# Kernel tuning notes

Hardware: AMD Instinct MI355X
Metric: run time of the kernel (lower is better)

## Reference

```python
import jax, jax.numpy as jnp
import numpy as np

H = 64  # latent_dim // 2


def _lstm_cell(x, h, c, Wih, Whh, b):
    # PyTorch gate order: i, f, g, o
    g = x @ Wih.T + h @ Whh.T + b
    i, f, gg, o = jnp.split(g, 4, axis=-1)
    c = jax.nn.sigmoid(f) * c + jax.nn.sigmoid(i) * jnp.tanh(gg)
    h = jax.nn.sigmoid(o) * jnp.tanh(c)
    return h, c


def _run_lstm(x, Wih, Whh, b):
    # x: [B, T, D] -> outputs [B, T, H], final h, c (zero-initialized state)
    B = x.shape[0]
    h0 = jnp.zeros((B, Whh.shape[1]), x.dtype)

    def step(carry, xt):
        h, c = _lstm_cell(xt, carry[0], carry[1], Wih, Whh, b)
        return (h, c), h

    (h, c), ys = jax.lax.scan(step, (h0, h0), jnp.swapaxes(x, 0, 1))
    return jnp.swapaxes(ys, 0, 1), h, c


def setup_inputs() -> dict:
    key = jax.random.key(0)
    ks = jax.random.split(key, 16)
    B, S, T, D = 512, 1024, 512, 3
    s = 1.0 / np.sqrt(H)

    def u(k, shape):
        return jax.random.uniform(k, shape, jnp.float32, -s, s)

    return {
        "src": jax.random.normal(ks[0], (B, S, D), jnp.float32),
        "trg": jax.random.normal(ks[1], (B, T, D), jnp.float32),
        "enc1_Wih": u(ks[2], (4 * H, D)),
        "enc1_Whh": u(ks[3], (4 * H, H)),
        "enc1_b": u(ks[4], (4 * H,)),
        "enc2_Wih": u(ks[5], (4 * H, H)),
        "enc2_Whh": u(ks[6], (4 * H, H)),
        "enc2_b": u(ks[7], (4 * H,)),
        "dec1_Wih": u(ks[8], (4 * H, D)),
        "dec1_Whh": u(ks[9], (4 * H, H)),
        "dec1_b": u(ks[10], (4 * H,)),
        "dec2_Wih": u(ks[11], (4 * H, H)),
        "dec2_Whh": u(ks[12], (4 * H, H)),
        "dec2_b": u(ks[13], (4 * H,)),
        "fc_W": u(ks[14], (D, H)),
        "fc_b": u(ks[15], (D,)),
    }


def reference(src, trg, enc1_Wih, enc1_Whh, enc1_b, enc2_Wih, enc2_Whh, enc2_b,
              dec1_Wih, dec1_Whh, dec1_b, dec2_Wih, dec2_Whh, dec2_b, fc_W, fc_b):
    # Encoder: two stacked LSTMs over src; keep final state of layer 2.
    y1, _, _ = _run_lstm(src, enc1_Wih, enc1_Whh, enc1_b)
    _, h, c = _run_lstm(y1, enc2_Wih, enc2_Whh, enc2_b)

    # Decoder (teacher_forcing_ratio = 1.0, the only well-defined branch):
    # at each step both decoder LSTMs share/chain the SAME (h, c) state,
    # exactly as the original Decoder.forward does with seq-len-1 inputs.
    def step(carry, xt):
        h, c = carry
        h1, c1 = _lstm_cell(xt, h, c, dec1_Wih, dec1_Whh, dec1_b)
        h2, c2 = _lstm_cell(h1, h1, c1, dec2_Wih, dec2_Whh, dec2_b)
        return (h2, c2), h2 @ fc_W.T + fc_b

    xs = jnp.swapaxes(trg[:, :-1, :], 0, 1)  # inputs for t = 1..T-1
    _, preds = jax.lax.scan(step, (h, c), xs)
    preds = jnp.swapaxes(preds, 0, 1)  # [B, T-1, 3]

    B = trg.shape[0]
    zero0 = jnp.zeros((B, 1, fc_b.shape[0]), preds.dtype)  # outputs[:, 0] stays 0
    return jnp.concatenate([zero0, preds], axis=1)
```

## Files before the change

### kernel.cpp

```cpp
#include <hip/hip_runtime.h>
#include <math.h>

typedef _Float16 f16;
typedef _Float16 f16x8 __attribute__((ext_vector_type(8)));
typedef float    f32x4 __attribute__((ext_vector_type(4)));

#define MFMA16(A, B, C) __builtin_amdgcn_mfma_f32_16x16x32_f16((A), (B), (C), 0, 0, 0)
#define LOG2E 1.44269504088896f

__device__ __forceinline__ float sig2(float a) {
    return __builtin_amdgcn_rcpf(1.0f + __builtin_amdgcn_exp2f(a));
}
__device__ __forceinline__ float tanh2(float c) {
    return fmaf(2.0f, sig2(c * (-2.0f * LOG2E)), -1.0f);
}

__device__ __forceinline__ f16x8 ldfrag(const float* __restrict__ W, int n, int k0, float s) {
    const float* p = W + (size_t)n * 64 + k0;
    f16x8 r;
#pragma unroll
    for (int j = 0; j < 8; j++) r[j] = (f16)(s * p[j]);
    return r;
}

__global__ __launch_bounds__(512, 2)
void seq2seq_kernel(const float* __restrict__ src, const float* __restrict__ trg,
                    const float* __restrict__ e1ih, const float* __restrict__ e1hh,
                    const float* __restrict__ e1b,
                    const float* __restrict__ e2ih, const float* __restrict__ e2hh,
                    const float* __restrict__ e2b,
                    const float* __restrict__ d1ih, const float* __restrict__ d1hh,
                    const float* __restrict__ d1b,
                    const float* __restrict__ d2ih, const float* __restrict__ d2hh,
                    const float* __restrict__ d2b,
                    const float* __restrict__ fcW, const float* __restrict__ fcb,
                    float* __restrict__ out)
{
    const int bp   = blockIdx.x;
    const int tid  = threadIdx.x;
    const int wv   = tid >> 6;
    const bool isB = (wv >= 4);
    const int wvg  = wv & 3;
    const int lane = tid & 63;
    const int quad = lane >> 4;
    const int c15  = lane & 15;
    const int u16  = wvg * 16 + c15;
    const int qb   = quad & 1;
    const int ab   = c15 & 1;

    __shared__ __align__(16) float xst[1024][8];
    __shared__ __align__(16) float tst[512][8];
    __shared__ __align__(16) f16 h1l[2][2][64];
    __shared__ __align__(16) f16 h2l[2][2][64];
    __shared__ float c1buf[2][64];
    __shared__ float c2buf[2][64];
    __shared__ __align__(16) f16 ring[2][16][72];

    {
        const float* s0 = src + (size_t)(2 * bp) * 3072;
        const float* s1 = s0 + 3072;
        for (int i = tid; i < 3072; i += 512) {
            int t = i / 3, c = i - 3 * t;
            xst[t][c]     = s0[i];
            xst[t][4 + c] = s1[i];
        }
        const float* t0p = trg + (size_t)(2 * bp) * 1536;
        const float* t1p = t0p + 1536;
        for (int i = tid; i < 1536; i += 512) {
            int t = i / 3, c = i - 3 * t;
            tst[t][c]     = t0p[i];
            tst[t][4 + c] = t1p[i];
        }
    }

    f16x8 E1hh[4][2];
    f16x8 E2ih[4][2], E2hh[4][2];
    float xw[4][3], bias1[4];
    f32x4 bs2[4];
    if (!isB) {
#pragma unroll
        for (int g = 0; g < 4; g++) {
            const float s = (g == 2) ? (-2.0f * LOG2E) : (-LOG2E);
            const int n = g * 64 + u16;
#pragma unroll
            for (int c = 0; c < 2; c++)
                E1hh[g][c] = ldfrag(e1hh, n, c * 32 + quad * 8, s);
            xw[g][0] = s * e1ih[n * 3 + 0];
            xw[g][1] = s * e1ih[n * 3 + 1];
            xw[g][2] = s * e1ih[n * 3 + 2];
            bias1[g] = s * e1b[n];
        }
    } else {
#pragma unroll
        for (int g = 0; g < 4; g++) {
            const float s = (g == 2) ? (-2.0f * LOG2E) : (-LOG2E);
            const int n = g * 64 + u16;
#pragma unroll
            for (int c = 0; c < 2; c++) {
                E2ih[g][c] = ldfrag(e2ih, n, c * 32 + quad * 8, s);
                E2hh[g][c] = ldfrag(e2hh, n, c * 32 + quad * 8, s);
            }
            float bv = s * e2b[n];
            bs2[g] = (f32x4){bv, bv, bv, bv};
        }
    }

    float c1 = 0.f, c2 = 0.f;
    if (tid < 256) {
        (&h1l[0][0][0])[tid] = (f16)0.f;
        (&h2l[0][0][0])[tid] = (f16)0.f;
    }
    __syncthreads();

    const f32x4 z4 = {0.f, 0.f, 0.f, 0.f};

    f32x4 xq = z4, xnq = z4;
    if (!isB) xq = *(const f32x4*)&xst[0][qb * 4];

#pragma unroll 1
    for (int tau = 0; tau <= 1024; tau++) {
        const int w = tau & 1;
        if (!isB) {
            if (tau < 1024) {
                const f16* h1p = h1l[w ^ 1][ab];
                f16x8 a0 = *(const f16x8*)(h1p + quad * 8);
                f16x8 a1 = *(const f16x8*)(h1p + 32 + quad * 8);
                float xt[4];
#pragma unroll
                for (int g = 0; g < 4; g++)
                    xt[g] = fmaf(xw[g][0], xq.x,
                            fmaf(xw[g][1], xq.y, fmaf(xw[g][2], xq.z, bias1[g])));
                f32x4 acc[4];
#pragma unroll
                for (int g = 0; g < 4; g++)
                    acc[g] = MFMA16(a1, E1hh[g][1], MFMA16(a0, E1hh[g][0], z4));
                float v[4];
#pragma unroll
                for (int g = 0; g < 4; g++)
                    v[g] = (qb ? acc[g][1] : acc[g][0]) + xt[g];
                float iv = sig2(v[0]), fv = sig2(v[1]);
                float gv = fmaf(2.0f, sig2(v[2]), -1.0f), ov = sig2(v[3]);
                c1 = fv * c1 + iv * gv;
                if (quad < 2) h1l[w][quad][u16] = (f16)(ov * tanh2(c1));
                const int tn = (tau + 1 < 1024) ? tau + 1 : 1023;
                xnq = *(const f32x4*)&xst[tn][qb * 4];
            }
        } else {
            if (tau > 0) {
                const f16* h1p = h1l[w ^ 1][ab];
                const f16* h2p = h2l[w ^ 1][ab];
                f16x8 a0 = *(const f16x8*)(h1p + quad * 8);
                f16x8 a1 = *(const f16x8*)(h1p + 32 + quad * 8);
                f16x8 b0 = *(const f16x8*)(h2p + quad * 8);
                f16x8 b1 = *(const f16x8*)(h2p + 32 + quad * 8);
                f32x4 accA[4], accB[4];
#pragma unroll
                for (int g = 0; g < 4; g++) {
                    accA[g] = MFMA16(a1, E2ih[g][1], MFMA16(a0, E2ih[g][0], bs2[g]));
                    accB[g] = MFMA16(b1, E2hh[g][1], MFMA16(b0, E2hh[g][0], z4));
                }
                float v[4];
#pragma unroll
                for (int g = 0; g < 4; g++)
                    v[g] = (qb ? accA[g][1] : accA[g][0]) +
                           (qb ? accB[g][1] : accB[g][0]);
                float iv = sig2(v[0]), fv = sig2(v[1]);
                float gv = fmaf(2.0f, sig2(v[2]), -1.0f), ov = sig2(v[3]);
                c2 = fv * c2 + iv * gv;
                if (quad < 2) h2l[w][quad][u16] = (f16)(ov * tanh2(c2));
            }
        }
        __syncthreads();
        if (!isB) xq = xnq;
    }

    f16x8 D1hh[4][2];
    f16x8 W2s[4][2];
    float dxw[4][3], db1[4];
    f32x4 db2s[4];
    if (!isB) {
#pragma unroll
        for (int g = 0; g < 4; g++) {
            const float s = (g == 2) ? (-2.0f * LOG2E) : (-LOG2E);
            const int n = g * 64 + u16;
#pragma unroll
            for (int c = 0; c < 2; c++)
                D1hh[g][c] = ldfrag(d1hh, n, c * 32 + quad * 8, s);
            dxw[g][0] = s * d1ih[n * 3 + 0];
            dxw[g][1] = s * d1ih[n * 3 + 1];
            dxw[g][2] = s * d1ih[n * 3 + 2];
            db1[g] = s * d1b[n];
        }
    } else {
#pragma unroll
        for (int g = 0; g < 4; g++) {
            const float s = (g == 2) ? (-2.0f * LOG2E) : (-LOG2E);
            const int n = g * 64 + u16;
#pragma unroll
            for (int c = 0; c < 2; c++) {
                const int k0 = c * 32 + quad * 8;
                const float* pa = d2ih + (size_t)n * 64 + k0;
                const float* pb = d2hh + (size_t)n * 64 + k0;
                f16x8 r;
#pragma unroll
                for (int j = 0; j < 8; j++) r[j] = (f16)(s * (pa[j] + pb[j]));
                W2s[g][c] = r;
            }
            float bv = s * d2b[n];
            db2s[g] = (f32x4){bv, bv, bv, bv};
        }
        if (quad < 2) c2buf[quad][u16] = c2;
    }
    f16x8 FW0 = {}, FW1 = {};
    float fb = 0.f;
    if (wv >= 6 && c15 < 3) {
#pragma unroll
        for (int j = 0; j < 8; j++) {
            FW0[j] = (f16)fcW[c15 * 64 + quad * 8 + j];
            FW1[j] = (f16)fcW[c15 * 64 + 32 + quad * 8 + j];
        }
        fb = fcb[c15];
    }
    __syncthreads();

    f32x4 tq = z4, tnq = z4;
    if (!isB) tq = *(const f32x4*)&tst[0][qb * 4];

#pragma unroll 1
    for (int t = 0; t < 511; t++) {
        const int r = t & 1, w = r ^ 1;
        if (!isB) {
            const f16* hp = h2l[r][ab];
            f16x8 a0 = *(const f16x8*)(hp + quad * 8);
            f16x8 a1 = *(const f16x8*)(hp + 32 + quad * 8);
            float cdin = c2buf[qb][u16];
            float xt[4];
#pragma unroll
            for (int g = 0; g < 4; g++)
                xt[g] = fmaf(dxw[g][0], tq.x,
                        fmaf(dxw[g][1], tq.y, fmaf(dxw[g][2], tq.z, db1[g])));
            f32x4 acc[4];
#pragma unroll
            for (int g = 0; g < 4; g++)
                acc[g] = MFMA16(a1, D1hh[g][1], MFMA16(a0, D1hh[g][0], z4));
            float v[4];
#pragma unroll
            for (int g = 0; g < 4; g++)
                v[g] = (qb ? acc[g][1] : acc[g][0]) + xt[g];
            float iv = sig2(v[0]), fv = sig2(v[1]);
            float gv = fmaf(2.0f, sig2(v[2]), -1.0f), ov = sig2(v[3]);
            float c1d = fv * cdin + iv * gv;
            if (quad < 2) {
                h1l[w][quad][u16] = (f16)(ov * tanh2(c1d));
                c1buf[quad][u16]  = c1d;
            }
            const int tn = (t + 1 < 511) ? t + 1 : 510;
            tnq = *(const f32x4*)&tst[tn][qb * 4];
        } else if (wv >= 6 && t > 0 && (t & 15) == 0) {
            const int bsel = wv - 6;
            const f16* rp = &ring[bsel][0][0];
            f16x8 fa0 = *(const f16x8*)(rp + c15 * 72 + quad * 8);
            f16x8 fa1 = *(const f16x8*)(rp + c15 * 72 + 32 + quad * 8);
            f32x4 acc = MFMA16(fa1, FW1, MFMA16(fa0, FW0, z4));
            if (c15 < 3) {
                float* ob = out + (((size_t)(2 * bp + bsel) * 512 + (t - 15)) * 3) + c15;
#pragma unroll
                for (int rg = 0; rg < 4; rg++)
                    ob[(quad * 4 + rg) * 3] = acc[rg] + fb;
            }
        }
        __syncthreads();
        if (!isB) tq = tnq;

        if (isB) {
            const f16* np = h1l[w][ab];
            f16x8 m0 = *(const f16x8*)(np + quad * 8);
            f16x8 m1 = *(const f16x8*)(np + 32 + quad * 8);
            float c1in = c1buf[qb][u16];
            f32x4 acc[4];
#pragma unroll
            for (int g = 0; g < 4; g++)
                acc[g] = MFMA16(m1, W2s[g][1], MFMA16(m0, W2s[g][0], db2s[g]));
            float v[4];
#pragma unroll
            for (int g = 0; g < 4; g++)
                v[g] = (qb ? acc[g][1] : acc[g][0]);
            float i2 = sig2(v[0]), f2 = sig2(v[1]);
            float g2 = fmaf(2.0f, sig2(v[2]), -1.0f), o2 = sig2(v[3]);
            float c2d = f2 * c1in + i2 * g2;
            if (quad < 2) {
                f16 hh = (f16)(o2 * tanh2(c2d));
                h2l[w][quad][u16] = hh;
                c2buf[quad][u16]  = c2d;
                ring[quad][t & 15][u16] = hh;
            }
        }
        __syncthreads();
    }

    if (wv >= 6) {
        const int bsel = wv - 6;
        const f16* rp = &ring[bsel][0][0];
        f16x8 fa0 = *(const f16x8*)(rp + c15 * 72 + quad * 8);
        f16x8 fa1 = *(const f16x8*)(rp + c15 * 72 + 32 + quad * 8);
        f32x4 acc = MFMA16(fa1, FW1, MFMA16(fa0, FW0, z4));
        if (c15 < 3) {
            float* ob = out + (((size_t)(2 * bp + bsel) * 512 + 497) * 3) + c15;
#pragma unroll
            for (int rg = 0; rg < 4; rg++) {
                int step = quad * 4 + rg;
                if (step < 15) ob[step * 3] = acc[rg] + fb;
            }
        }
    }
}

extern "C" void kernel_launch(void* const* d_in, const int* in_sizes, int n_in,
                              void* d_out, int out_size, void* d_ws, size_t ws_size,
                              hipStream_t stream)
{
    const float* src   = (const float*)d_in[0];
    const float* trg   = (const float*)d_in[1];
    const float* e1ih  = (const float*)d_in[2];
    const float* e1hh  = (const float*)d_in[3];
    const float* e1b   = (const float*)d_in[4];
    const float* e2ih  = (const float*)d_in[5];
    const float* e2hh  = (const float*)d_in[6];
    const float* e2b   = (const float*)d_in[7];
    const float* dd1ih = (const float*)d_in[8];
    const float* dd1hh = (const float*)d_in[9];
    const float* dd1b  = (const float*)d_in[10];
    const float* dd2ih = (const float*)d_in[11];
    const float* dd2hh = (const float*)d_in[12];
    const float* dd2b  = (const float*)d_in[13];
    const float* fcW   = (const float*)d_in[14];
    const float* fcb   = (const float*)d_in[15];
    float* out = (float*)d_out;

    hipMemsetAsync(d_out, 0, (size_t)out_size * sizeof(float), stream);

    seq2seq_kernel<<<256, 512, 0, stream>>>(src, trg,
                                            e1ih, e1hh, e1b, e2ih, e2hh, e2b,
                                            dd1ih, dd1hh, dd1b, dd2ih, dd2hh, dd2b,
                                            fcW, fcb, out);
}
```

Baseline: 832.3 us.

## Move encoder layer-2 input projection to layer-1 waves via shared-memory pipeline

Encoder layer-1 waves now also compute the layer-2 input projection (h1 times E2ih) and pass it to the layer-2 waves through a double-buffered shared buffer. This adds one pipeline stage and one extra loop iteration. Layer-2 waves then run only the recurrent MFMAs, which balances the per-step work between the two wave groups and shortens the critical path per barrier. Launch bounds drop to one block per SM to give room for the extra register fragments, and the h2 buffer parity in the decoder is flipped to match the new final write index.

```diff
diff --git a/kernel.cpp b/kernel.cpp
--- a/kernel.cpp
+++ b/kernel.cpp
@@ -23,7 +23,7 @@
     return r;
 }
 
-__global__ __launch_bounds__(512, 2)
+__global__ __launch_bounds__(512, 1)
 void seq2seq_kernel(const float* __restrict__ src, const float* __restrict__ trg,
                     const float* __restrict__ e1ih, const float* __restrict__ e1hh,
                     const float* __restrict__ e1b,
@@ -55,6 +55,7 @@
     __shared__ float c1buf[2][64];
     __shared__ float c2buf[2][64];
     __shared__ __align__(16) f16 ring[2][16][72];
+    __shared__ __align__(16) float prj[2][2][64][4];
 
     {
         const float* s0 = src + (size_t)(2 * bp) * 3072;
@@ -73,8 +74,8 @@
         }
     }
 
-    f16x8 E1hh[4][2];
-    f16x8 E2ih[4][2], E2hh[4][2];
+    f16x8 E1hh[4][2], E2ih[4][2];
+    f16x8 E2hh[4][2];
     float xw[4][3], bias1[4];
     f32x4 bs2[4];
     if (!isB) {
@@ -83,8 +84,10 @@
             const float s = (g == 2) ? (-2.0f * LOG2E) : (-LOG2E);
             const int n = g * 64 + u16;
 #pragma unroll
-            for (int c = 0; c < 2; c++)
+            for (int c = 0; c < 2; c++) {
                 E1hh[g][c] = ldfrag(e1hh, n, c * 32 + quad * 8, s);
+                E2ih[g][c] = ldfrag(e2ih, n, c * 32 + quad * 8, s);
+            }
             xw[g][0] = s * e1ih[n * 3 + 0];
             xw[g][1] = s * e1ih[n * 3 + 1];
             xw[g][2] = s * e1ih[n * 3 + 2];
@@ -96,10 +99,8 @@
             const float s = (g == 2) ? (-2.0f * LOG2E) : (-LOG2E);
             const int n = g * 64 + u16;
 #pragma unroll
-            for (int c = 0; c < 2; c++) {
-                E2ih[g][c] = ldfrag(e2ih, n, c * 32 + quad * 8, s);
+            for (int c = 0; c < 2; c++)
                 E2hh[g][c] = ldfrag(e2hh, n, c * 32 + quad * 8, s);
-            }
             float bv = s * e2b[n];
             bs2[g] = (f32x4){bv, bv, bv, bv};
         }
@@ -118,56 +119,65 @@
     if (!isB) xq = *(const f32x4*)&xst[0][qb * 4];
 
 #pragma unroll 1
-    for (int tau = 0; tau <= 1024; tau++) {
-        const int w = tau & 1;
+    for (int tau = 0; tau <= 1025; tau++) {
         if (!isB) {
-            if (tau < 1024) {
-                const f16* h1p = h1l[w ^ 1][ab];
+            if (tau <= 1024) {
+                const f16* h1p = h1l[(tau + 1) & 1][ab];
                 f16x8 a0 = *(const f16x8*)(h1p + quad * 8);
                 f16x8 a1 = *(const f16x8*)(h1p + 32 + quad * 8);
-                float xt[4];
-#pragma unroll
-                for (int g = 0; g < 4; g++)
-                    xt[g] = fmaf(xw[g][0], xq.x,
-                            fmaf(xw[g][1], xq.y, fmaf(xw[g][2], xq.z, bias1[g])));
-                f32x4 acc[4];
-#pragma unroll
-                for (int g = 0; g < 4; g++)
-                    acc[g] = MFMA16(a1, E1hh[g][1], MFMA16(a0, E1hh[g][0], z4));
-                float v[4];
-#pragma unroll
-                for (int g = 0; g < 4; g++)
-                    v[g] = (qb ? acc[g][1] : acc[g][0]) + xt[g];
-                float iv = sig2(v[0]), fv = sig2(v[1]);
-                float gv = fmaf(2.0f, sig2(v[2]), -1.0f), ov = sig2(v[3]);
-                c1 = fv * c1 + iv * gv;
-                if (quad < 2) h1l[w][quad][u16] = (f16)(ov * tanh2(c1));
-                const int tn = (tau + 1 < 1024) ? tau + 1 : 1023;
-                xnq = *(const f32x4*)&xst[tn][qb * 4];
+                if (tau < 1024) {
+                    float xt[4];
+#pragma unroll
+                    for (int g = 0; g < 4; g++)
+                        xt[g] = fmaf(xw[g][0], xq.x,
+                                fmaf(xw[g][1], xq.y, fmaf(xw[g][2], xq.z, bias1[g])));
+                    f32x4 acc[4];
+#pragma unroll
+                    for (int g = 0; g < 4; g++)
+                        acc[g] = MFMA16(a1, E1hh[g][1], MFMA16(a0, E1hh[g][0], z4));
+                    float v[4];
+#pragma unroll
+                    for (int g = 0; g < 4; g++)
+                        v[g] = (qb ? acc[g][1] : acc[g][0]) + xt[g];
+                    float iv = sig2(v[0]), fv = sig2(v[1]);
+                    float gv = fmaf(2.0f, sig2(v[2]), -1.0f), ov = sig2(v[3]);
+                    c1 = fv * c1 + iv * gv;
+                    if (quad < 2) h1l[tau & 1][quad][u16] = (f16)(ov * tanh2(c1));
+                    const int tn = (tau + 1 < 1024) ? tau + 1 : 1023;
+                    xnq = *(const f32x4*)&xst[tn][qb * 4];
+                }
+                if (tau >= 1) {
+                    f32x4 ap[4];
+#pragma unroll
+                    for (int g = 0; g < 4; g++)
+                        ap[g] = MFMA16(a1, E2ih[g][1], MFMA16(a0, E2ih[g][0], z4));
+                    if (quad < 2) {
+                        f32x4 pv;
+#pragma unroll
+                        for (int g = 0; g < 4; g++)
+                            pv[g] = qb ? ap[g][1] : ap[g][0];
+                        *(f32x4*)&prj[(tau + 1) & 1][qb][u16][0] = pv;
+                    }
+                }
             }
         } else {
-            if (tau > 0) {
-                const f16* h1p = h1l[w ^ 1][ab];
-                const f16* h2p = h2l[w ^ 1][ab];
-                f16x8 a0 = *(const f16x8*)(h1p + quad * 8);
-                f16x8 a1 = *(const f16x8*)(h1p + 32 + quad * 8);
+            if (tau >= 2) {
+                const f16* h2p = h2l[(tau + 1) & 1][ab];
+                f32x4 pj = *(const f32x4*)&prj[tau & 1][qb][u16][0];
                 f16x8 b0 = *(const f16x8*)(h2p + quad * 8);
                 f16x8 b1 = *(const f16x8*)(h2p + 32 + quad * 8);
-                f32x4 accA[4], accB[4];
-#pragma unroll
-                for (int g = 0; g < 4; g++) {
-                    accA[g] = MFMA16(a1, E2ih[g][1], MFMA16(a0, E2ih[g][0], bs2[g]));
-                    accB[g] = MFMA16(b1, E2hh[g][1], MFMA16(b0, E2hh[g][0], z4));
-                }
+                f32x4 accB[4];
+#pragma unroll
+                for (int g = 0; g < 4; g++)
+                    accB[g] = MFMA16(b1, E2hh[g][1], MFMA16(b0, E2hh[g][0], bs2[g]));
                 float v[4];
 #pragma unroll
                 for (int g = 0; g < 4; g++)
-                    v[g] = (qb ? accA[g][1] : accA[g][0]) +
-                           (qb ? accB[g][1] : accB[g][0]);
+                    v[g] = pj[g] + (qb ? accB[g][1] : accB[g][0]);
                 float iv = sig2(v[0]), fv = sig2(v[1]);
                 float gv = fmaf(2.0f, sig2(v[2]), -1.0f), ov = sig2(v[3]);
                 c2 = fv * c2 + iv * gv;
-                if (quad < 2) h2l[w][quad][u16] = (f16)(ov * tanh2(c2));
+                if (quad < 2) h2l[tau & 1][quad][u16] = (f16)(ov * tanh2(c2));
             }
         }
         __syncthreads();
@@ -201,10 +211,10 @@
                 const int k0 = c * 32 + quad * 8;
                 const float* pa = d2ih + (size_t)n * 64 + k0;
                 const float* pb = d2hh + (size_t)n * 64 + k0;
-                f16x8 r;
-#pragma unroll
-                for (int j = 0; j < 8; j++) r[j] = (f16)(s * (pa[j] + pb[j]));
-                W2s[g][c] = r;
+                f16x8 r2;
+#pragma unroll
+                for (int j = 0; j < 8; j++) r2[j] = (f16)(s * (pa[j] + pb[j]));
+                W2s[g][c] = r2;
             }
             float bv = s * d2b[n];
             db2s[g] = (f32x4){bv, bv, bv, bv};
@@ -230,7 +240,7 @@
     for (int t = 0; t < 511; t++) {
         const int r = t & 1, w = r ^ 1;
         if (!isB) {
-            const f16* hp = h2l[r][ab];
+            const f16* hp = h2l[w][ab];
             f16x8 a0 = *(const f16x8*)(hp + quad * 8);
             f16x8 a1 = *(const f16x8*)(hp + 32 + quad * 8);
             float cdin = c2buf[qb][u16];
@@ -290,7 +300,7 @@
             float c2d = f2 * c1in + i2 * g2;
             if (quad < 2) {
                 f16 hh = (f16)(o2 * tanh2(c2d));
-                h2l[w][quad][u16] = hh;
+                h2l[r][quad][u16] = hh;
                 c2buf[quad][u16]  = c2d;
                 ring[quad][t & 15][u16] = hh;
             }
```

Result: no change. 829.1 us, median of 2 (-0.4%).
